# Kernel tuning notes

Hardware: AMD Instinct MI355X
Metric: run time of the kernel (lower is better)

Reference implementation:

```python
import jax, jax.numpy as jnp
import numpy as np
from jax import lax

H = 64  # LSTM units (hard-coded in the module)


def _lstm(x, W, U, b, return_sequences):
    """Keras-style LSTM (inference; recurrent_dropout inactive).
    x: [B, T, F]; W: [F, 4H]; U: [H, 4H]; b: [4H].
    Gate order (Keras): i, f, g(cell), o.
    """
    B = x.shape[0]
    # Precompute input contribution for all timesteps: [T, B, 4H]
    xz = jnp.einsum('btf,fg->tbg', x, W) + b

    def step(carry, z_t):
        h, c = carry
        z = z_t + h @ U  # [B, 4H]
        i = jax.nn.sigmoid(z[:, :H])
        f = jax.nn.sigmoid(z[:, H:2 * H])
        g = jnp.tanh(z[:, 2 * H:3 * H])
        o = jax.nn.sigmoid(z[:, 3 * H:])
        c = f * c + i * g
        h = o * jnp.tanh(c)
        return (h, c), h

    init = (jnp.zeros((B, H), x.dtype), jnp.zeros((B, H), x.dtype))
    (h_last, _), hs = lax.scan(step, init, xz)
    if return_sequences:
        return jnp.transpose(hs, (1, 0, 2))  # [B, T, H]
    return h_last  # [B, H]


def setup_inputs() -> dict:
    key = jax.random.key(0)
    ks = jax.random.split(key, 8)
    B, T, F = 4096, 256, 32
    s_in = 1.0 / np.sqrt(F)
    s_h = 1.0 / np.sqrt(H)
    return {
        'x': jax.random.normal(ks[0], (B, T, F), jnp.float32),
        'W1': jax.random.normal(ks[1], (F, 4 * H), jnp.float32) * s_in,
        'U1': jax.random.normal(ks[2], (H, 4 * H), jnp.float32) * s_h,
        'b1': jnp.zeros((4 * H,), jnp.float32),
        'W2': jax.random.normal(ks[3], (H, 4 * H), jnp.float32) * s_h,
        'U2': jax.random.normal(ks[4], (H, 4 * H), jnp.float32) * s_h,
        'b2': jnp.zeros((4 * H,), jnp.float32),
        'Wd': jax.random.normal(ks[5], (H, H), jnp.float32) * s_h,
        'bd': jnp.zeros((H,), jnp.float32),
        'Wo': jax.random.normal(ks[6], (H, 1), jnp.float32) * s_h,
        'bo': jnp.zeros((1,), jnp.float32),
    }


def reference(x, W1, U1, b1, W2, U2, b2, Wd, bd, Wo, bo):
    h_seq = _lstm(x, W1, U1, b1, return_sequences=True)   # hidden_lstm
    h_last = _lstm(h_seq, W2, U2, b2, return_sequences=False)  # lstm_layer
    d = jax.nn.sigmoid(h_last @ Wd + bd)  # Dense(64, sigmoid)
    return jax.nn.sigmoid(d @ Wo + bo)    # Dense(1, sigmoid) -> [B, 1]
```

## Files before the change

kernel.cpp:

```cpp
#include <hip/hip_runtime.h>


typedef __attribute__((ext_vector_type(8))) short short8;
typedef __attribute__((ext_vector_type(4))) float floatx4;
typedef __attribute__((ext_vector_type(2))) float floatx2;

__device__ __forceinline__ float ex2(float x){ return __builtin_amdgcn_exp2f(x); }
__device__ __forceinline__ float rcp_(float x){ return __builtin_amdgcn_rcpf(x); }
__device__ __forceinline__ float sigm(float x){ return rcp_(1.0f + ex2(-1.44269504f*x)); }
__device__ __forceinline__ unsigned bfbits(float f){
    unsigned u = __builtin_bit_cast(unsigned, f);
    u += 0x7FFFu + ((u >> 16) & 1u);
    return u >> 16;
}
__device__ __forceinline__ short f2bf(float f){ return (short)bfbits(f); }
__device__ __forceinline__ unsigned pack_bf2(float a, float b){
    return bfbits(a) | (bfbits(b) << 16);
}

#define MFMA_BF16 __builtin_amdgcn_mfma_f32_16x16x32_bf16

__global__ __launch_bounds__(1024, 1)
void lstm2_tz(const float* __restrict__ x,
              const float* __restrict__ W1, const float* __restrict__ U1, const float* __restrict__ b1,
              const float* __restrict__ W2, const float* __restrict__ U2, const float* __restrict__ b2,
              const float* __restrict__ Wd, const float* __restrict__ bd,
              const float* __restrict__ Wo, const float* __restrict__ bo,
              float* __restrict__ out)
{
    __shared__ __align__(16) short h1b[2][16 * 72];
    __shared__ __align__(16) short h2b[2][16 * 72];
    __shared__ __align__(16) short xsb[2][16 * 40];
    __shared__ float psum[4][16];

    const int tid  = threadIdx.x;
    const int w    = tid >> 6;
    const bool isL1 = (w < 8);
    const int wv   = isL1 ? w : (w - 8);
    const int lane = tid & 63;
    const int n    = lane & 15;
    const int q    = lane >> 4;
    const int b0   = blockIdx.x * 16;

    const float LG = 1.44269504f;

    const int ugl = n >> 2;
    const int gA  = n & 3;
    const float sA = (gA == 2) ? (2.0f * LG) : (-LG);

    short8  Wa[8];
    floatx4 bC[2];
    if (isL1) {
#pragma unroll
        for (int tt = 0; tt < 2; ++tt) {
            const int t = wv * 2 + tt;
            const int ncol = gA * 64 + t * 4 + ugl;
#pragma unroll
            for (int j = 0; j < 8; ++j) {
                const int k = q * 8 + j;
                Wa[tt * 3 + 0][j] = f2bf(W1[k * 256 + ncol] * sA);
                Wa[tt * 3 + 1][j] = f2bf(U1[k * 256 + ncol] * sA);
                Wa[tt * 3 + 2][j] = f2bf(U1[(32 + k) * 256 + ncol] * sA);
            }
#pragma unroll
            for (int r = 0; r < 4; ++r)
                bC[tt][r] = b1[r * 64 + t * 4 + q] * ((r == 2) ? (2.0f * LG) : (-LG));
        }
    } else {
#pragma unroll
        for (int tt = 0; tt < 2; ++tt) {
            const int t = wv * 2 + tt;
            const int ncol = gA * 64 + t * 4 + ugl;
#pragma unroll
            for (int j = 0; j < 8; ++j) {
                const int k = q * 8 + j;
                Wa[tt * 4 + 0][j] = f2bf(W2[k * 256 + ncol] * sA);
                Wa[tt * 4 + 1][j] = f2bf(W2[(32 + k) * 256 + ncol] * sA);
                Wa[tt * 4 + 2][j] = f2bf(U2[k * 256 + ncol] * sA);
                Wa[tt * 4 + 3][j] = f2bf(U2[(32 + k) * 256 + ncol] * sA);
            }
#pragma unroll
            for (int r = 0; r < 4; ++r)
                bC[tt][r] = b2[r * 64 + t * 4 + q] * ((r == 2) ? (2.0f * LG) : (-LG));
        }
    }

    {
        unsigned* p1 = (unsigned*)&h1b[0][0];
        unsigned* p2 = (unsigned*)&h2b[0][0];
        for (int i = tid; i < 1152; i += 1024) { p1[i] = 0u; p2[i] = 0u; }
    }

    const int xr = tid >> 4;
    const int xc = (tid & 15) * 2;
    const float* xrow = x + (size_t)(b0 + xr) * 8192 + xc;
    floatx2 xv0;
    if (tid < 256) {
        floatx2 v = *(const floatx2*)xrow;
        *(unsigned*)&xsb[0][xr * 40 + xc] = pack_bf2(v.x, v.y);
        xv0 = *(const floatx2*)(xrow + 32);
    }
    __syncthreads();

    float c[2] = {0, 0};

    for (int u = 0; u <= 256; ++u) {
        const int par = u & 1, pax = par ^ 1;
        if (isL1) {
            if (u < 256) {
                short8 bx  = *(const short8*)&xsb[par][n * 40 + q * 8];
                short8 bh0 = *(const short8*)&h1b[pax][n * 72 + q * 8];
                short8 bh1 = *(const short8*)&h1b[pax][n * 72 + 32 + q * 8];
#pragma unroll
                for (int tt = 0; tt < 2; ++tt) {
                    floatx4 z = bC[tt];
                    z = MFMA_BF16(Wa[tt * 3 + 0], bx,  z, 0, 0, 0);
                    z = MFMA_BF16(Wa[tt * 3 + 1], bh0, z, 0, 0, 0);
                    z = MFMA_BF16(Wa[tt * 3 + 2], bh1, z, 0, 0, 0);
                    float iv = rcp_(1.0f + ex2(z[0]));
                    float fv = rcp_(1.0f + ex2(z[1]));
                    float rg = rcp_(1.0f + ex2(z[2]));
                    float ov = rcp_(1.0f + ex2(z[3]));
                    float gp = fmaf(-5.77078016f, rg, 2.88539008f);
                    c[tt] = fmaf(fv, c[tt], iv * gp);
                    float th = fmaf(-2.0f, rcp_(1.0f + ex2(c[tt])), 1.0f);
                    h1b[par][n * 72 + (wv * 2 + tt) * 4 + q] = f2bf(ov * th);
                }
                if (tid < 256 && u < 255) {
                    *(unsigned*)&xsb[pax][xr * 40 + xc] = pack_bf2(xv0.x, xv0.y);
                    if (u < 254) xv0 = *(const floatx2*)(xrow + (size_t)(u + 2) * 32);
                }
            }
        } else {
            if (u >= 1) {
                short8 bh0 = *(const short8*)&h1b[pax][n * 72 + q * 8];
                short8 bh1 = *(const short8*)&h1b[pax][n * 72 + 32 + q * 8];
                short8 bg0 = *(const short8*)&h2b[par][n * 72 + q * 8];
                short8 bg1 = *(const short8*)&h2b[par][n * 72 + 32 + q * 8];
#pragma unroll
                for (int tt = 0; tt < 2; ++tt) {
                    floatx4 z = bC[tt];
                    z = MFMA_BF16(Wa[tt * 4 + 0], bh0, z, 0, 0, 0);
                    z = MFMA_BF16(Wa[tt * 4 + 1], bh1, z, 0, 0, 0);
                    z = MFMA_BF16(Wa[tt * 4 + 2], bg0, z, 0, 0, 0);
                    z = MFMA_BF16(Wa[tt * 4 + 3], bg1, z, 0, 0, 0);
                    float iv = rcp_(1.0f + ex2(z[0]));
                    float fv = rcp_(1.0f + ex2(z[1]));
                    float rg = rcp_(1.0f + ex2(z[2]));
                    float ov = rcp_(1.0f + ex2(z[3]));
                    float gp = fmaf(-5.77078016f, rg, 2.88539008f);
                    c[tt] = fmaf(fv, c[tt], iv * gp);
                    float th = fmaf(-2.0f, rcp_(1.0f + ex2(c[tt])), 1.0f);
                    h2b[pax][n * 72 + (wv * 2 + tt) * 4 + q] = f2bf(ov * th);
                }
            }
        }
        __syncthreads();
    }

    if (!isL1 && wv < 4) {
        const int colD = wv * 16 + n;
        short8 wd0, wd1;
#pragma unroll
        for (int j = 0; j < 8; ++j) {
            wd0[j] = f2bf(Wd[(q * 8 + j) * 64 + colD] * (-LG));
            wd1[j] = f2bf(Wd[(32 + q * 8 + j) * 64 + colD] * (-LG));
        }
        short8 hA0 = *(const short8*)&h2b[1][n * 72 + q * 8];
        short8 hA1 = *(const short8*)&h2b[1][n * 72 + 32 + q * 8];
        const float bdv = bd[colD] * (-LG);
        floatx4 dacc = { bdv, bdv, bdv, bdv };
        dacc = MFMA_BF16(hA0, wd0, dacc, 0, 0, 0);
        dacc = MFMA_BF16(hA1, wd1, dacc, 0, 0, 0);
        const float wo = Wo[colD];
#pragma unroll
        for (int r = 0; r < 4; ++r) {
            float p = rcp_(1.0f + ex2(dacc[r])) * wo;
            p += __shfl_xor(p, 1, 64);
            p += __shfl_xor(p, 2, 64);
            p += __shfl_xor(p, 4, 64);
            p += __shfl_xor(p, 8, 64);
            if (n == 0) psum[wv][q * 4 + r] = p;
        }
    }
    __syncthreads();
    if (tid < 16) {
        float s = psum[0][tid] + psum[1][tid] + psum[2][tid] + psum[3][tid] + bo[0];
        out[b0 + tid] = sigm(s);
    }
}

extern "C" void kernel_launch(void* const* d_in, const int* in_sizes, int n_in,
                              void* d_out, int out_size, void* d_ws, size_t ws_size,
                              hipStream_t stream) {
    (void)in_sizes; (void)n_in; (void)d_ws; (void)ws_size; (void)out_size;
    const float* x  = (const float*)d_in[0];
    const float* W1 = (const float*)d_in[1];
    const float* U1 = (const float*)d_in[2];
    const float* b1 = (const float*)d_in[3];
    const float* W2 = (const float*)d_in[4];
    const float* U2 = (const float*)d_in[5];
    const float* b2 = (const float*)d_in[6];
    const float* Wd = (const float*)d_in[7];
    const float* bd = (const float*)d_in[8];
    const float* Wo = (const float*)d_in[9];
    const float* bo = (const float*)d_in[10];
    lstm2_tz<<<dim3(256), dim3(1024), 0, stream>>>(
        x, W1, U1, b1, W2, U2, b2, Wd, bd, Wo, bo, (float*)d_out);
}
```

Baseline: 343.7 us.

## Give every wave one tile of both LSTM layers instead of splitting waves by layer

Before, waves 0-7 ran layer 1 and waves 8-15 ran layer 2, each handling two gate tiles. Now all 16 waves each handle one tile of layer 1 and one tile of layer 2 in the same step, with a peeled prologue and epilogue for the one-step skew. This balances the work per wave (layer 2 has more MFMAs than layer 1) and lets each wave interleave two independent MFMA and transcendental chains to hide latency. The exponentials in the cell update are also grouped ahead of the reciprocals. Each wave now holds seven weight fragments, the same register count as before.

```diff
diff --git a/kernel.cpp b/kernel.cpp
--- a/kernel.cpp
+++ b/kernel.cpp
@@ -20,23 +20,34 @@
 
 #define MFMA_BF16 __builtin_amdgcn_mfma_f32_16x16x32_bf16
 
+#define CELL(zv, cc, wptr) do {                                          \
+    float e0 = ex2((zv)[0]), e1 = ex2((zv)[1]);                          \
+    float e2 = ex2((zv)[2]), e3 = ex2((zv)[3]);                          \
+    float iv = rcp_(1.0f + e0);                                          \
+    float fv = rcp_(1.0f + e1);                                          \
+    float rg = rcp_(1.0f + e2);                                          \
+    float ov = rcp_(1.0f + e3);                                          \
+    float gp = fmaf(-5.77078016f, rg, 2.88539008f);    \
+    (cc) = fmaf(fv, (cc), iv * gp);                                      \
+    float th = fmaf(-2.0f, rcp_(1.0f + ex2(cc)), 1.0f);                  \
+    *(wptr) = f2bf(ov * th);                                             \
+} while (0)
+
 __global__ __launch_bounds__(1024, 1)
-void lstm2_tz(const float* __restrict__ x,
-              const float* __restrict__ W1, const float* __restrict__ U1, const float* __restrict__ b1,
-              const float* __restrict__ W2, const float* __restrict__ U2, const float* __restrict__ b2,
-              const float* __restrict__ Wd, const float* __restrict__ bd,
-              const float* __restrict__ Wo, const float* __restrict__ bo,
-              float* __restrict__ out)
+void lstm2_uni(const float* __restrict__ x,
+               const float* __restrict__ W1, const float* __restrict__ U1, const float* __restrict__ b1,
+               const float* __restrict__ W2, const float* __restrict__ U2, const float* __restrict__ b2,
+               const float* __restrict__ Wd, const float* __restrict__ bd,
+               const float* __restrict__ Wo, const float* __restrict__ bo,
+               float* __restrict__ out)
 {
-    __shared__ __align__(16) short h1b[2][16 * 72];
-    __shared__ __align__(16) short h2b[2][16 * 72];
-    __shared__ __align__(16) short xsb[2][16 * 40];
+    __shared__ __align__(16) short h1s[2 * 1152];
+    __shared__ __align__(16) short h2s[2 * 1152];
+    __shared__ __align__(16) short xss[2 * 640];
     __shared__ float psum[4][16];
 
     const int tid  = threadIdx.x;
     const int w    = tid >> 6;
-    const bool isL1 = (w < 8);
-    const int wv   = isL1 ? w : (w - 8);
     const int lane = tid & 63;
     const int n    = lane & 15;
     const int q    = lane >> 4;
@@ -47,48 +58,31 @@
     const int ugl = n >> 2;
     const int gA  = n & 3;
     const float sA = (gA == 2) ? (2.0f * LG) : (-LG);
-
-    short8  Wa[8];
-    floatx4 bC[2];
-    if (isL1) {
-#pragma unroll
-        for (int tt = 0; tt < 2; ++tt) {
-            const int t = wv * 2 + tt;
-            const int ncol = gA * 64 + t * 4 + ugl;
-#pragma unroll
-            for (int j = 0; j < 8; ++j) {
-                const int k = q * 8 + j;
-                Wa[tt * 3 + 0][j] = f2bf(W1[k * 256 + ncol] * sA);
-                Wa[tt * 3 + 1][j] = f2bf(U1[k * 256 + ncol] * sA);
-                Wa[tt * 3 + 2][j] = f2bf(U1[(32 + k) * 256 + ncol] * sA);
-            }
-#pragma unroll
-            for (int r = 0; r < 4; ++r)
-                bC[tt][r] = b1[r * 64 + t * 4 + q] * ((r == 2) ? (2.0f * LG) : (-LG));
-        }
-    } else {
-#pragma unroll
-        for (int tt = 0; tt < 2; ++tt) {
-            const int t = wv * 2 + tt;
-            const int ncol = gA * 64 + t * 4 + ugl;
-#pragma unroll
-            for (int j = 0; j < 8; ++j) {
-                const int k = q * 8 + j;
-                Wa[tt * 4 + 0][j] = f2bf(W2[k * 256 + ncol] * sA);
-                Wa[tt * 4 + 1][j] = f2bf(W2[(32 + k) * 256 + ncol] * sA);
-                Wa[tt * 4 + 2][j] = f2bf(U2[k * 256 + ncol] * sA);
-                Wa[tt * 4 + 3][j] = f2bf(U2[(32 + k) * 256 + ncol] * sA);
-            }
-#pragma unroll
-            for (int r = 0; r < 4; ++r)
-                bC[tt][r] = b2[r * 64 + t * 4 + q] * ((r == 2) ? (2.0f * LG) : (-LG));
-        }
-    }
-
-    {
-        unsigned* p1 = (unsigned*)&h1b[0][0];
-        unsigned* p2 = (unsigned*)&h2b[0][0];
-        for (int i = tid; i < 1152; i += 1024) { p1[i] = 0u; p2[i] = 0u; }
+    const int ncol = gA * 64 + w * 4 + ugl;
+
+    short8  Wa1[3], Wa2[4];
+    floatx4 bC1, bC2;
+#pragma unroll
+    for (int j = 0; j < 8; ++j) {
+        const int k = q * 8 + j;
+        Wa1[0][j] = f2bf(W1[k * 256 + ncol] * sA);
+        Wa1[1][j] = f2bf(U1[k * 256 + ncol] * sA);
+        Wa1[2][j] = f2bf(U1[(32 + k) * 256 + ncol] * sA);
+        Wa2[0][j] = f2bf(W2[k * 256 + ncol] * sA);
+        Wa2[1][j] = f2bf(W2[(32 + k) * 256 + ncol] * sA);
+        Wa2[2][j] = f2bf(U2[k * 256 + ncol] * sA);
+        Wa2[3][j] = f2bf(U2[(32 + k) * 256 + ncol] * sA);
+    }
+#pragma unroll
+    for (int r = 0; r < 4; ++r) {
+        const float sr = (r == 2) ? (2.0f * LG) : (-LG);
+        bC1[r] = b1[r * 64 + w * 4 + q] * sr;
+        bC2[r] = b2[r * 64 + w * 4 + q] * sr;
+    }
+
+    if (tid < 576) {
+        ((unsigned*)(h1s + 1152))[tid] = 0u;
+        ((unsigned*)(h2s + 1152))[tid] = 0u;
     }
 
     const int xr = tid >> 4;
@@ -97,68 +91,84 @@
     floatx2 xv0;
     if (tid < 256) {
         floatx2 v = *(const floatx2*)xrow;
-        *(unsigned*)&xsb[0][xr * 40 + xc] = pack_bf2(v.x, v.y);
+        *(unsigned*)&xss[xr * 40 + xc] = pack_bf2(v.x, v.y);
         xv0 = *(const floatx2*)(xrow + 32);
     }
     __syncthreads();
 
-    float c[2] = {0, 0};
-
-    for (int u = 0; u <= 256; ++u) {
-        const int par = u & 1, pax = par ^ 1;
-        if (isL1) {
-            if (u < 256) {
-                short8 bx  = *(const short8*)&xsb[par][n * 40 + q * 8];
-                short8 bh0 = *(const short8*)&h1b[pax][n * 72 + q * 8];
-                short8 bh1 = *(const short8*)&h1b[pax][n * 72 + 32 + q * 8];
-#pragma unroll
-                for (int tt = 0; tt < 2; ++tt) {
-                    floatx4 z = bC[tt];
-                    z = MFMA_BF16(Wa[tt * 3 + 0], bx,  z, 0, 0, 0);
-                    z = MFMA_BF16(Wa[tt * 3 + 1], bh0, z, 0, 0, 0);
-                    z = MFMA_BF16(Wa[tt * 3 + 2], bh1, z, 0, 0, 0);
-                    float iv = rcp_(1.0f + ex2(z[0]));
-                    float fv = rcp_(1.0f + ex2(z[1]));
-                    float rg = rcp_(1.0f + ex2(z[2]));
-                    float ov = rcp_(1.0f + ex2(z[3]));
-                    float gp = fmaf(-5.77078016f, rg, 2.88539008f);
-                    c[tt] = fmaf(fv, c[tt], iv * gp);
-                    float th = fmaf(-2.0f, rcp_(1.0f + ex2(c[tt])), 1.0f);
-                    h1b[par][n * 72 + (wv * 2 + tt) * 4 + q] = f2bf(ov * th);
-                }
-                if (tid < 256 && u < 255) {
-                    *(unsigned*)&xsb[pax][xr * 40 + xc] = pack_bf2(xv0.x, xv0.y);
-                    if (u < 254) xv0 = *(const floatx2*)(xrow + (size_t)(u + 2) * 32);
-                }
-            }
-        } else {
-            if (u >= 1) {
-                short8 bh0 = *(const short8*)&h1b[pax][n * 72 + q * 8];
-                short8 bh1 = *(const short8*)&h1b[pax][n * 72 + 32 + q * 8];
-                short8 bg0 = *(const short8*)&h2b[par][n * 72 + q * 8];
-                short8 bg1 = *(const short8*)&h2b[par][n * 72 + 32 + q * 8];
-#pragma unroll
-                for (int tt = 0; tt < 2; ++tt) {
-                    floatx4 z = bC[tt];
-                    z = MFMA_BF16(Wa[tt * 4 + 0], bh0, z, 0, 0, 0);
-                    z = MFMA_BF16(Wa[tt * 4 + 1], bh1, z, 0, 0, 0);
-                    z = MFMA_BF16(Wa[tt * 4 + 2], bg0, z, 0, 0, 0);
-                    z = MFMA_BF16(Wa[tt * 4 + 3], bg1, z, 0, 0, 0);
-                    float iv = rcp_(1.0f + ex2(z[0]));
-                    float fv = rcp_(1.0f + ex2(z[1]));
-                    float rg = rcp_(1.0f + ex2(z[2]));
-                    float ov = rcp_(1.0f + ex2(z[3]));
-                    float gp = fmaf(-5.77078016f, rg, 2.88539008f);
-                    c[tt] = fmaf(fv, c[tt], iv * gp);
-                    float th = fmaf(-2.0f, rcp_(1.0f + ex2(c[tt])), 1.0f);
-                    h2b[pax][n * 72 + (wv * 2 + tt) * 4 + q] = f2bf(ov * th);
-                }
-            }
+    const int rdA = n * 72 + q * 8;
+    const int rdB = rdA + 32;
+    const int rdX = n * 40 + q * 8;
+    const int wrH = n * 72 + w * 4 + q;
+
+    float c1 = 0.0f, c2 = 0.0f;
+
+    {
+        short8 bx  = *(const short8*)&xss[rdX];
+        short8 h1a = *(const short8*)&h1s[1152 + rdA];
+        short8 h1c = *(const short8*)&h1s[1152 + rdB];
+        floatx4 z1 = bC1;
+        z1 = MFMA_BF16(Wa1[0], bx,  z1, 0, 0, 0);
+        z1 = MFMA_BF16(Wa1[1], h1a, z1, 0, 0, 0);
+        z1 = MFMA_BF16(Wa1[2], h1c, z1, 0, 0, 0);
+        CELL(z1, c1, &h1s[0 + wrH]);
+        if (tid < 256) {
+            *(unsigned*)&xss[640 + xr * 40 + xc] = pack_bf2(xv0.x, xv0.y);
+            xv0 = *(const floatx2*)(xrow + 64);
         }
         __syncthreads();
     }
 
-    if (!isL1 && wv < 4) {
+    for (int k = 1; k < 256; ++k) {
+        const int par = k & 1, pax = par ^ 1;
+        const int oR  = pax * 1152;
+        const int oW1 = par * 1152;
+        const int oR2 = par * 1152;
+        const int oW2 = pax * 1152;
+        const int oX  = par * 640;
+
+        short8 bx  = *(const short8*)&xss[oX + rdX];
+        short8 h1a = *(const short8*)&h1s[oR + rdA];
+        short8 h1c = *(const short8*)&h1s[oR + rdB];
+        short8 h2a = *(const short8*)&h2s[oR2 + rdA];
+        short8 h2c = *(const short8*)&h2s[oR2 + rdB];
+
+        floatx4 z1 = bC1;
+        z1 = MFMA_BF16(Wa1[0], bx,  z1, 0, 0, 0);
+        z1 = MFMA_BF16(Wa1[1], h1a, z1, 0, 0, 0);
+        z1 = MFMA_BF16(Wa1[2], h1c, z1, 0, 0, 0);
+        floatx4 z2 = bC2;
+        z2 = MFMA_BF16(Wa2[0], h1a, z2, 0, 0, 0);
+        z2 = MFMA_BF16(Wa2[1], h1c, z2, 0, 0, 0);
+        z2 = MFMA_BF16(Wa2[2], h2a, z2, 0, 0, 0);
+        z2 = MFMA_BF16(Wa2[3], h2c, z2, 0, 0, 0);
+
+        CELL(z1, c1, &h1s[oW1 + wrH]);
+        CELL(z2, c2, &h2s[oW2 + wrH]);
+
+        if (tid < 256 && k < 255) {
+            *(unsigned*)&xss[pax * 640 + xr * 40 + xc] = pack_bf2(xv0.x, xv0.y);
+            if (k < 254) xv0 = *(const floatx2*)(xrow + (size_t)(k + 2) * 32);
+        }
+        __syncthreads();
+    }
+
+    {
+        short8 h1a = *(const short8*)&h1s[1152 + rdA];
+        short8 h1c = *(const short8*)&h1s[1152 + rdB];
+        short8 h2a = *(const short8*)&h2s[0 + rdA];
+        short8 h2c = *(const short8*)&h2s[0 + rdB];
+        floatx4 z2 = bC2;
+        z2 = MFMA_BF16(Wa2[0], h1a, z2, 0, 0, 0);
+        z2 = MFMA_BF16(Wa2[1], h1c, z2, 0, 0, 0);
+        z2 = MFMA_BF16(Wa2[2], h2a, z2, 0, 0, 0);
+        z2 = MFMA_BF16(Wa2[3], h2c, z2, 0, 0, 0);
+        CELL(z2, c2, &h2s[1152 + wrH]);
+        __syncthreads();
+    }
+
+    if (w >= 8 && w < 12) {
+        const int wv = w - 8;
         const int colD = wv * 16 + n;
         short8 wd0, wd1;
 #pragma unroll
@@ -166,8 +176,8 @@
             wd0[j] = f2bf(Wd[(q * 8 + j) * 64 + colD] * (-LG));
             wd1[j] = f2bf(Wd[(32 + q * 8 + j) * 64 + colD] * (-LG));
         }
-        short8 hA0 = *(const short8*)&h2b[1][n * 72 + q * 8];
-        short8 hA1 = *(const short8*)&h2b[1][n * 72 + 32 + q * 8];
+        short8 hA0 = *(const short8*)&h2s[1152 + rdA];
+        short8 hA1 = *(const short8*)&h2s[1152 + rdB];
         const float bdv = bd[colD] * (-LG);
         floatx4 dacc = { bdv, bdv, bdv, bdv };
         dacc = MFMA_BF16(hA0, wd0, dacc, 0, 0, 0);
@@ -205,6 +215,6 @@
     const float* bd = (const float*)d_in[8];
     const float* Wo = (const float*)d_in[9];
     const float* bo = (const float*)d_in[10];
-    lstm2_tz<<<dim3(256), dim3(1024), 0, stream>>>(
+    lstm2_uni<<<dim3(256), dim3(1024), 0, stream>>>(
         x, W1, U1, b1, W2, U2, b2, Wd, bd, Wo, bo, (float*)d_out);
 }
```

Result: slower. 368.9 us (+7.3%).

## Triple-buffer x staging, prefetch x fragment, pack h stores via lane shuffle

Applied to the files above, without the earlier changes.

Moves the x tile staging to a triple-buffered LDS ring filled by half of each layer-1 wave, so the next timestep's x fragment is loaded into registers before the barrier. Hidden-state writes now pair adjacent values through a cross-lane shuffle, so half the lanes issue one 32-bit LDS store instead of every lane issuing a 16-bit store. Bf16 packing switches to the HIP intrinsic conversion. The intent is to cut LDS traffic and the x-load latency on the serial recurrence path, at the cost of an extra shuffle per cell and more LDS.

```diff
diff --git a/kernel.cpp b/kernel.cpp
--- a/kernel.cpp
+++ b/kernel.cpp
@@ -1,4 +1,5 @@
 #include <hip/hip_runtime.h>
+#include <hip/hip_bf16.h>
 
 
 typedef __attribute__((ext_vector_type(8))) short short8;
@@ -15,22 +16,36 @@
 }
 __device__ __forceinline__ short f2bf(float f){ return (short)bfbits(f); }
 __device__ __forceinline__ unsigned pack_bf2(float a, float b){
-    return bfbits(a) | (bfbits(b) << 16);
+    float2 t; t.x = a; t.y = b;
+    __hip_bfloat162 p = __float22bfloat162_rn(t);
+    unsigned r; __builtin_memcpy(&r, &p, 4);
+    return r;
 }
 
 #define MFMA_BF16 __builtin_amdgcn_mfma_f32_16x16x32_bf16
 
+__device__ __forceinline__ float cellh(const floatx4& z, float& c){
+    float iv = rcp_(1.0f + ex2(z[0]));
+    float fv = rcp_(1.0f + ex2(z[1]));
+    float rg = rcp_(1.0f + ex2(z[2]));
+    float ov = rcp_(1.0f + ex2(z[3]));
+    float gp = fmaf(-5.77078016f, rg, 2.88539008f);
+    c = fmaf(fv, c, iv * gp);
+    float th = fmaf(-2.0f, rcp_(1.0f + ex2(c)), 1.0f);
+    return ov * th;
+}
+
 __global__ __launch_bounds__(1024, 1)
-void lstm2_tz(const float* __restrict__ x,
-              const float* __restrict__ W1, const float* __restrict__ U1, const float* __restrict__ b1,
-              const float* __restrict__ W2, const float* __restrict__ U2, const float* __restrict__ b2,
-              const float* __restrict__ Wd, const float* __restrict__ bd,
-              const float* __restrict__ Wo, const float* __restrict__ bo,
-              float* __restrict__ out)
+void lstm2_tz2(const float* __restrict__ x,
+               const float* __restrict__ W1, const float* __restrict__ U1, const float* __restrict__ b1,
+               const float* __restrict__ W2, const float* __restrict__ U2, const float* __restrict__ b2,
+               const float* __restrict__ Wd, const float* __restrict__ bd,
+               const float* __restrict__ Wo, const float* __restrict__ bo,
+               float* __restrict__ out)
 {
-    __shared__ __align__(16) short h1b[2][16 * 72];
-    __shared__ __align__(16) short h2b[2][16 * 72];
-    __shared__ __align__(16) short xsb[2][16 * 40];
+    __shared__ __align__(16) short h1s[2 * 1152];
+    __shared__ __align__(16) short h2s[2 * 1152];
+    __shared__ __align__(16) short xss[3 * 640];
     __shared__ float psum[4][16];
 
     const int tid  = threadIdx.x;
@@ -86,57 +101,65 @@
     }
 
     {
-        unsigned* p1 = (unsigned*)&h1b[0][0];
-        unsigned* p2 = (unsigned*)&h2b[0][0];
+        unsigned* p1 = (unsigned*)&h1s[0];
+        unsigned* p2 = (unsigned*)&h2s[0];
         for (int i = tid; i < 1152; i += 1024) { p1[i] = 0u; p2[i] = 0u; }
     }
 
-    const int xr = tid >> 4;
-    const int xc = (tid & 15) * 2;
-    const float* xrow = x + (size_t)(b0 + xr) * 8192 + xc;
+    const int srow = wv * 2 + q;
+    const int scol = (lane & 15) * 2;
+    const float* xp = x + (size_t)(b0 + srow) * 8192 + scol;
+    const bool stager = isL1 && (lane < 32);
     floatx2 xv0;
-    if (tid < 256) {
-        floatx2 v = *(const floatx2*)xrow;
-        *(unsigned*)&xsb[0][xr * 40 + xc] = pack_bf2(v.x, v.y);
-        xv0 = *(const floatx2*)(xrow + 32);
+    if (stager) {
+        floatx2 v0 = *(const floatx2*)xp;
+        floatx2 v1 = *(const floatx2*)(xp + 32);
+        *(unsigned*)&xss[0   + srow * 40 + scol] = pack_bf2(v0.x, v0.y);
+        *(unsigned*)&xss[640 + srow * 40 + scol] = pack_bf2(v1.x, v1.y);
+        xv0 = *(const floatx2*)(xp + 64);
     }
     __syncthreads();
 
+    const int rdA = n * 72 + q * 8;
+    const int rdB = rdA + 32;
+    const int rdX = n * 40 + q * 8;
+
     float c[2] = {0, 0};
+    int xb0 = 0, xb1 = 1, xb2 = 2;
+
+    short8 bx_cur;
+    if (isL1) bx_cur = *(const short8*)&xss[rdX];
 
     for (int u = 0; u <= 256; ++u) {
         const int par = u & 1, pax = par ^ 1;
         if (isL1) {
             if (u < 256) {
-                short8 bx  = *(const short8*)&xsb[par][n * 40 + q * 8];
-                short8 bh0 = *(const short8*)&h1b[pax][n * 72 + q * 8];
-                short8 bh1 = *(const short8*)&h1b[pax][n * 72 + 32 + q * 8];
+                short8 h1a = *(const short8*)&h1s[pax * 1152 + rdA];
+                short8 h1c = *(const short8*)&h1s[pax * 1152 + rdB];
 #pragma unroll
                 for (int tt = 0; tt < 2; ++tt) {
                     floatx4 z = bC[tt];
-                    z = MFMA_BF16(Wa[tt * 3 + 0], bx,  z, 0, 0, 0);
-                    z = MFMA_BF16(Wa[tt * 3 + 1], bh0, z, 0, 0, 0);
-                    z = MFMA_BF16(Wa[tt * 3 + 2], bh1, z, 0, 0, 0);
-                    float iv = rcp_(1.0f + ex2(z[0]));
-                    float fv = rcp_(1.0f + ex2(z[1]));
-                    float rg = rcp_(1.0f + ex2(z[2]));
-                    float ov = rcp_(1.0f + ex2(z[3]));
-                    float gp = fmaf(-5.77078016f, rg, 2.88539008f);
-                    c[tt] = fmaf(fv, c[tt], iv * gp);
-                    float th = fmaf(-2.0f, rcp_(1.0f + ex2(c[tt])), 1.0f);
-                    h1b[par][n * 72 + (wv * 2 + tt) * 4 + q] = f2bf(ov * th);
+                    z = MFMA_BF16(Wa[tt * 3 + 0], bx_cur, z, 0, 0, 0);
+                    z = MFMA_BF16(Wa[tt * 3 + 1], h1a,    z, 0, 0, 0);
+                    z = MFMA_BF16(Wa[tt * 3 + 2], h1c,    z, 0, 0, 0);
+                    float hv = cellh(z, c[tt]);
+                    float hp = __shfl_xor(hv, 16, 64);
+                    if (!(q & 1))
+                        *(unsigned*)&h1s[par * 1152 + n * 72 + (wv * 2 + tt) * 4 + q]
+                            = pack_bf2(hv, hp);
                 }
-                if (tid < 256 && u < 255) {
-                    *(unsigned*)&xsb[pax][xr * 40 + xc] = pack_bf2(xv0.x, xv0.y);
-                    if (u < 254) xv0 = *(const floatx2*)(xrow + (size_t)(u + 2) * 32);
+                if (stager && u < 254) {
+                    *(unsigned*)&xss[xb2 * 640 + srow * 40 + scol] = pack_bf2(xv0.x, xv0.y);
+                    if (u < 253) xv0 = *(const floatx2*)(xp + (size_t)(u + 3) * 32);
                 }
+                if (u < 255) bx_cur = *(const short8*)&xss[xb1 * 640 + rdX];
             }
         } else {
             if (u >= 1) {
-                short8 bh0 = *(const short8*)&h1b[pax][n * 72 + q * 8];
-                short8 bh1 = *(const short8*)&h1b[pax][n * 72 + 32 + q * 8];
-                short8 bg0 = *(const short8*)&h2b[par][n * 72 + q * 8];
-                short8 bg1 = *(const short8*)&h2b[par][n * 72 + 32 + q * 8];
+                short8 bh0 = *(const short8*)&h1s[pax * 1152 + rdA];
+                short8 bh1 = *(const short8*)&h1s[pax * 1152 + rdB];
+                short8 bg0 = *(const short8*)&h2s[par * 1152 + rdA];
+                short8 bg1 = *(const short8*)&h2s[par * 1152 + rdB];
 #pragma unroll
                 for (int tt = 0; tt < 2; ++tt) {
                     floatx4 z = bC[tt];
@@ -144,17 +167,15 @@
                     z = MFMA_BF16(Wa[tt * 4 + 1], bh1, z, 0, 0, 0);
                     z = MFMA_BF16(Wa[tt * 4 + 2], bg0, z, 0, 0, 0);
                     z = MFMA_BF16(Wa[tt * 4 + 3], bg1, z, 0, 0, 0);
-                    float iv = rcp_(1.0f + ex2(z[0]));
-                    float fv = rcp_(1.0f + ex2(z[1]));
-                    float rg = rcp_(1.0f + ex2(z[2]));
-                    float ov = rcp_(1.0f + ex2(z[3]));
-                    float gp = fmaf(-5.77078016f, rg, 2.88539008f);
-                    c[tt] = fmaf(fv, c[tt], iv * gp);
-                    float th = fmaf(-2.0f, rcp_(1.0f + ex2(c[tt])), 1.0f);
-                    h2b[pax][n * 72 + (wv * 2 + tt) * 4 + q] = f2bf(ov * th);
+                    float hv = cellh(z, c[tt]);
+                    float hp = __shfl_xor(hv, 16, 64);
+                    if (!(q & 1))
+                        *(unsigned*)&h2s[pax * 1152 + n * 72 + (wv * 2 + tt) * 4 + q]
+                            = pack_bf2(hv, hp);
                 }
             }
         }
+        { int t0 = xb0; xb0 = xb1; xb1 = xb2; xb2 = t0; }
         __syncthreads();
     }
 
@@ -166,8 +187,8 @@
             wd0[j] = f2bf(Wd[(q * 8 + j) * 64 + colD] * (-LG));
             wd1[j] = f2bf(Wd[(32 + q * 8 + j) * 64 + colD] * (-LG));
         }
-        short8 hA0 = *(const short8*)&h2b[1][n * 72 + q * 8];
-        short8 hA1 = *(const short8*)&h2b[1][n * 72 + 32 + q * 8];
+        short8 hA0 = *(const short8*)&h2s[1152 + rdA];
+        short8 hA1 = *(const short8*)&h2s[1152 + rdB];
         const float bdv = bd[colD] * (-LG);
         floatx4 dacc = { bdv, bdv, bdv, bdv };
         dacc = MFMA_BF16(hA0, wd0, dacc, 0, 0, 0);
@@ -205,6 +226,6 @@
     const float* bd = (const float*)d_in[8];
     const float* Wo = (const float*)d_in[9];
     const float* bo = (const float*)d_in[10];
-    lstm2_tz<<<dim3(256), dim3(1024), 0, stream>>>(
+    lstm2_tz2<<<dim3(256), dim3(1024), 0, stream>>>(
         x, W1, U1, b1, W2, U2, b2, Wd, bd, Wo, bo, (float*)d_out);
 }
```

Measured after the change: 388.0 us. 12.9% more time.
